# Performance work log

Hardware: AMD Instinct MI355X
Metric: run time of the kernel (lower is better)

The kernel has to match this reference:

```python
import jax, jax.numpy as jnp
import numpy as np

# FP8 E4M3 format constants
FP8_MAX = 448.0          # largest representable magnitude in E4M3
MANT_BITS = 3            # mantissa bits
_TINY = 2.0 ** -24


def fp8_fake_quant(x):
    """Per-tensor dynamic-scale FP8 (E4M3) fake quantization with STE.

    amax tracking (single-entry history on first call) -> scale = FP8_MAX/amax,
    scale, clamp to format range, round mantissa to MANT_BITS, dequantize.
    """
    amax = jax.lax.stop_gradient(jnp.max(jnp.abs(x)))
    scale = FP8_MAX / jnp.maximum(amax, _TINY)
    xs = jnp.clip(x * scale, -FP8_MAX, FP8_MAX)
    a = jnp.abs(xs)
    # exponent of each value; floor(log2) gives the binade, lsb is the quantum
    e = jnp.floor(jnp.log2(jnp.maximum(a, _TINY)))
    lsb = jnp.exp2(e - MANT_BITS)
    q = jnp.round(xs / lsb) * lsb
    q = jnp.where(a == 0.0, 0.0, q) / scale
    # straight-through estimator: forward q, backward identity
    return x + jax.lax.stop_gradient(q - x)


def setup_inputs() -> dict:
    key = jax.random.key(0)
    k1, k2, k3 = jax.random.split(key, 3)
    tokens, d_in, d_out = 4096, 4096, 16384
    x = jax.random.normal(k1, (tokens, d_in), dtype=jnp.float32)
    weight = jax.random.normal(k2, (d_out, d_in), dtype=jnp.float32) * 0.02
    bias = jax.random.normal(k3, (d_out,), dtype=jnp.float32) * 0.02
    return {"x": x, "weight": weight, "bias": bias}


def reference(x, weight, bias):
    qw = fp8_fake_quant(weight)          # quantize weights
    qx = fp8_fake_quant(x)               # quantize_input=True
    # F.linear: x @ W^T + b
    return jnp.einsum("ti,oi->to", qx, qw) + bias
```

## Files before the change

### kernel.cpp

```cpp
#include <hip/hip_runtime.h>
#include <hip/hip_bf16.h>


typedef __attribute__((ext_vector_type(8))) __bf16 bf16x8;
typedef __attribute__((ext_vector_type(4))) float f32x4;
typedef __attribute__((ext_vector_type(4))) unsigned int u32x4;

#define FP8_MAX 448.0f
#define TINY 5.9604644775390625e-8f

__device__ __forceinline__ void gload_lds16(const void* g, void* l) {
  __builtin_amdgcn_global_load_lds(
      (__attribute__((address_space(1))) void*)g,
      (__attribute__((address_space(3))) void*)l, 16, 0, 0);
}

__global__ __launch_bounds__(256) void amax_kernel(
    const float* __restrict__ in, long n, unsigned* __restrict__ out) {
  long i0 = (long)blockIdx.x * blockDim.x + threadIdx.x;
  long stride = (long)gridDim.x * blockDim.x;
  long n4 = n >> 2;
  const float4* in4 = (const float4*)in;
  float m = 0.f;
  for (long i = i0; i < n4; i += stride) {
    float4 v = in4[i];
    m = fmaxf(m, fmaxf(fmaxf(fabsf(v.x), fabsf(v.y)),
                       fmaxf(fabsf(v.z), fabsf(v.w))));
  }
  #pragma unroll
  for (int off = 32; off > 0; off >>= 1)
    m = fmaxf(m, __shfl_xor(m, off, 64));
  __shared__ float red[4];
  int lane = threadIdx.x & 63, wid = threadIdx.x >> 6;
  if (lane == 0) red[wid] = m;
  __syncthreads();
  if (threadIdx.x == 0) {
    m = fmaxf(fmaxf(red[0], red[1]), fmaxf(red[2], red[3]));
    atomicMax(out, __float_as_uint(m));
  }
}

__device__ __forceinline__ unsigned fq1(float x, float s) {
  float xs = x * s;
  xs = fminf(fmaxf(xs, -FP8_MAX), FP8_MAX);
  unsigned u = __float_as_uint(xs);
  unsigned sign = u & 0x80000000u;
  unsigned mag = u & 0x7fffffffu;
  unsigned r = (mag + 0x7FFFFu + ((mag >> 20) & 1u)) & 0xFFF00000u;
  return (sign | r) >> 16;
}

__global__ __launch_bounds__(256) void quant_kernel(
    const float* __restrict__ in, unsigned short* __restrict__ out,
    const unsigned* __restrict__ amaxp, long n) {
  float s = FP8_MAX / fmaxf(__uint_as_float(*amaxp), TINY);
  long i0 = (long)blockIdx.x * blockDim.x + threadIdx.x;
  long stride = (long)gridDim.x * blockDim.x;
  long n8 = n >> 3;
  const float4* in4 = (const float4*)in;
  u32x4* out8 = (u32x4*)out;
  for (long i = i0; i < n8; i += stride) {
    float4 v0 = in4[2 * i];
    float4 v1 = in4[2 * i + 1];
    u32x4 o;
    o.x = fq1(v0.x, s) | (fq1(v0.y, s) << 16);
    o.y = fq1(v0.z, s) | (fq1(v0.w, s) << 16);
    o.z = fq1(v1.x, s) | (fq1(v1.y, s) << 16);
    o.w = fq1(v1.z, s) | (fq1(v1.w, s) << 16);
    out8[i] = o;
  }
}

__global__ __launch_bounds__(512, 2) void gemm_kernel(
    const unsigned short* __restrict__ qx, const unsigned short* __restrict__ qw,
    const float* __restrict__ bias, const unsigned* __restrict__ amaxp,
    float* __restrict__ out, int M, int N, int K) {
  __shared__ unsigned short As[2][2][256 * 32];
  __shared__ unsigned short Bs[2][2][256 * 32];

  const int tid = threadIdx.x;
  const int lane = tid & 63;
  const int wid = tid >> 6;
  const int wr = wid >> 2;
  const int wc = wid & 3;

  const int nbn = N >> 8;
  const int cpx = gridDim.x >> 3;
  const int swz = (blockIdx.x & 7) * cpx + (blockIdx.x >> 3);
  const int bm0 = (swz / nbn) << 8;
  const int bn0 = (swz % nbn) << 8;

  f32x4 acc[8][4] = {};

  const int srow = tid >> 2;
  const int scb = ((tid & 3) * 16) ^ ((srow & 3) << 4);
  const size_t a_off = (size_t)(bm0 + srow) * K + (scb >> 1);
  const size_t b_off = (size_t)(bn0 + srow) * K + (scb >> 1);
  const size_t jstride = (size_t)128 * K;
  const int ldsb = wid * 1024;

  const int rcb = (((lane >> 4) << 4) ^ ((lane & 3) << 4)) >> 1;
  const int arb = (wr * 128 + (lane & 15)) * 32 + rcb;
  const int brb = (wc * 64 + (lane & 15)) * 32 + rcb;

#define STAGE(d, kh, kt)                                                   \
  {                                                                        \
    const unsigned short* ga = qx + a_off + (kt) + (kh) * 32;              \
    const unsigned short* gb = qw + b_off + (kt) + (kh) * 32;              \
    char* la = (char*)&As[d][kh][0] + ldsb;                                \
    char* lb = (char*)&Bs[d][kh][0] + ldsb;                                \
    gload_lds16(ga, la);                                                   \
    gload_lds16(ga + jstride, la + 8192);                                  \
    gload_lds16(gb, lb);                                                   \
    gload_lds16(gb + jstride, lb + 8192);                                  \
  }

#define PHASE(d, kh)                                                       \
  {                                                                        \
    bf16x8 a[8], b[4];                                                     \
    _Pragma("unroll")                                                      \
    for (int m = 0; m < 8; ++m)                                            \
      a[m] = __builtin_bit_cast(bf16x8,                                    \
                *(const u32x4*)&As[d][kh][arb + m * 512]);                 \
    _Pragma("unroll")                                                      \
    for (int n = 0; n < 4; ++n)                                            \
      b[n] = __builtin_bit_cast(bf16x8,                                    \
                *(const u32x4*)&Bs[d][kh][brb + n * 512]);                 \
    __builtin_amdgcn_s_setprio(1);                                         \
    _Pragma("unroll")                                                      \
    for (int m = 0; m < 8; ++m)                                            \
      _Pragma("unroll")                                                    \
      for (int n = 0; n < 4; ++n)                                          \
        acc[m][n] = __builtin_amdgcn_mfma_f32_16x16x32_bf16(               \
            a[m], b[n], acc[m][n], 0, 0, 0);                               \
    __builtin_amdgcn_s_setprio(0);                                         \
  }

  STAGE(0, 0, 0);
  STAGE(0, 1, 0);

  const int nt = K >> 6;
  int cur = 0;
  for (int t = 0; t < nt; ++t) {
    const int ktn = (t + 1 == nt) ? 0 : ((t + 1) << 6);
    STAGE(cur ^ 1, 0, ktn);
    asm volatile("s_waitcnt vmcnt(8)" ::: "memory");
    __builtin_amdgcn_s_barrier();
    PHASE(cur, 0);
    STAGE(cur ^ 1, 1, ktn);
    asm volatile("s_waitcnt vmcnt(8)" ::: "memory");
    __builtin_amdgcn_s_barrier();
    PHASE(cur, 1);
    __builtin_amdgcn_s_barrier();
    cur ^= 1;
  }

  const float ax = fmaxf(__uint_as_float(amaxp[0]), TINY);
  const float aw = fmaxf(__uint_as_float(amaxp[1]), TINY);
  const float inv = ax * aw * (1.0f / (FP8_MAX * FP8_MAX));
  const int col0 = bn0 + wc * 64 + (lane & 15);
  const int row0 = bm0 + wr * 128 + ((lane >> 4) << 2);
  #pragma unroll
  for (int n = 0; n < 4; ++n) {
    float bv = bias[col0 + n * 16];
    #pragma unroll
    for (int m = 0; m < 8; ++m)
      #pragma unroll
      for (int j = 0; j < 4; ++j)
        out[(size_t)(row0 + m * 16 + j) * N + col0 + n * 16] =
            acc[m][n][j] * inv + bv;
  }
#undef STAGE
#undef PHASE
}

extern "C" void kernel_launch(void* const* d_in, const int* in_sizes, int n_in,
                              void* d_out, int out_size, void* d_ws, size_t ws_size,
                              hipStream_t stream) {
  const float* x = (const float*)d_in[0];
  const float* w = (const float*)d_in[1];
  const float* bias = (const float*)d_in[2];
  float* out = (float*)d_out;

  long nx = in_sizes[0];
  long nw = in_sizes[1];
  int N = in_sizes[2];
  int K = (int)(nw / N);
  int M = (int)(nx / K);

  unsigned* amax = (unsigned*)d_ws;
  unsigned short* qx = (unsigned short*)((char*)d_ws + 256);
  unsigned short* qw = (unsigned short*)((char*)d_ws + 256 + (size_t)M * K * 2);

  hipMemsetAsync(d_ws, 0, 256, stream);
  amax_kernel<<<2048, 256, 0, stream>>>(x, nx, amax + 0);
  amax_kernel<<<2048, 256, 0, stream>>>(w, nw, amax + 1);
  quant_kernel<<<4096, 256, 0, stream>>>(x, qx, amax + 0, nx);
  quant_kernel<<<4096, 256, 0, stream>>>(w, qw, amax + 1, nw);

  int nwg = (M >> 8) * (N >> 8);
  gemm_kernel<<<nwg, 512, 0, stream>>>(qx, qw, bias, amax, out, M, N, K);
}
```

Measured before the change: 1.210 ms.

## Retune LDS XOR swizzle, drop trailing loop barrier, merge amax and quant launches

```diff
diff --git a/kernel.cpp b/kernel.cpp
--- a/kernel.cpp
+++ b/kernel.cpp
@@ -16,10 +16,19 @@
 }
 
 __global__ __launch_bounds__(256) void amax_kernel(
-    const float* __restrict__ in, long n, unsigned* __restrict__ out) {
-  long i0 = (long)blockIdx.x * blockDim.x + threadIdx.x;
-  long stride = (long)gridDim.x * blockDim.x;
-  long n4 = n >> 2;
+    const float* __restrict__ x, long nx, const float* __restrict__ w, long nw,
+    unsigned* __restrict__ out) {
+  const int xblocks = 512;
+  const float* in;
+  long n4;
+  int bid, nb, slot;
+  if (blockIdx.x < xblocks) {
+    in = x; n4 = nx >> 2; bid = blockIdx.x; nb = xblocks; slot = 0;
+  } else {
+    in = w; n4 = nw >> 2; bid = blockIdx.x - xblocks; nb = gridDim.x - xblocks; slot = 1;
+  }
+  long i0 = (long)bid * blockDim.x + threadIdx.x;
+  long stride = (long)nb * blockDim.x;
   const float4* in4 = (const float4*)in;
   float m = 0.f;
   for (long i = i0; i < n4; i += stride) {
@@ -36,7 +45,7 @@
   __syncthreads();
   if (threadIdx.x == 0) {
     m = fmaxf(fmaxf(red[0], red[1]), fmaxf(red[2], red[3]));
-    atomicMax(out, __float_as_uint(m));
+    atomicMax(out + slot, __float_as_uint(m));
   }
 }
 
@@ -51,12 +60,20 @@
 }
 
 __global__ __launch_bounds__(256) void quant_kernel(
-    const float* __restrict__ in, unsigned short* __restrict__ out,
-    const unsigned* __restrict__ amaxp, long n) {
-  float s = FP8_MAX / fmaxf(__uint_as_float(*amaxp), TINY);
-  long i0 = (long)blockIdx.x * blockDim.x + threadIdx.x;
-  long stride = (long)gridDim.x * blockDim.x;
-  long n8 = n >> 3;
+    const float* __restrict__ x, unsigned short* __restrict__ qx, long nx,
+    const float* __restrict__ w, unsigned short* __restrict__ qw, long nw,
+    const unsigned* __restrict__ amaxp) {
+  const int xblocks = 1024;
+  const float* in; unsigned short* out; long n8; int bid, nb, slot;
+  if (blockIdx.x < xblocks) {
+    in = x; out = qx; n8 = nx >> 3; bid = blockIdx.x; nb = xblocks; slot = 0;
+  } else {
+    in = w; out = qw; n8 = nw >> 3; bid = blockIdx.x - xblocks;
+    nb = gridDim.x - xblocks; slot = 1;
+  }
+  float s = FP8_MAX / fmaxf(__uint_as_float(amaxp[slot]), TINY);
+  long i0 = (long)bid * blockDim.x + threadIdx.x;
+  long stride = (long)nb * blockDim.x;
   const float4* in4 = (const float4*)in;
   u32x4* out8 = (u32x4*)out;
   for (long i = i0; i < n8; i += stride) {
@@ -93,13 +110,13 @@
   f32x4 acc[8][4] = {};
 
   const int srow = tid >> 2;
-  const int scb = ((tid & 3) * 16) ^ ((srow & 3) << 4);
+  const int scb = ((tid & 3) ^ ((srow >> 1) & 3)) << 4;
   const size_t a_off = (size_t)(bm0 + srow) * K + (scb >> 1);
   const size_t b_off = (size_t)(bn0 + srow) * K + (scb >> 1);
   const size_t jstride = (size_t)128 * K;
   const int ldsb = wid * 1024;
 
-  const int rcb = (((lane >> 4) << 4) ^ ((lane & 3) << 4)) >> 1;
+  const int rcb = ((((lane >> 4) ^ ((lane >> 1) & 3)) << 4) >> 1);
   const int arb = (wr * 128 + (lane & 15)) * 32 + rcb;
   const int brb = (wc * 64 + (lane & 15)) * 32 + rcb;
 
@@ -151,7 +168,6 @@
     asm volatile("s_waitcnt vmcnt(8)" ::: "memory");
     __builtin_amdgcn_s_barrier();
     PHASE(cur, 1);
-    __builtin_amdgcn_s_barrier();
     cur ^= 1;
   }
 
@@ -193,10 +209,8 @@
   unsigned short* qw = (unsigned short*)((char*)d_ws + 256 + (size_t)M * K * 2);
 
   hipMemsetAsync(d_ws, 0, 256, stream);
-  amax_kernel<<<2048, 256, 0, stream>>>(x, nx, amax + 0);
-  amax_kernel<<<2048, 256, 0, stream>>>(w, nw, amax + 1);
-  quant_kernel<<<4096, 256, 0, stream>>>(x, qx, amax + 0, nx);
-  quant_kernel<<<4096, 256, 0, stream>>>(w, qw, amax + 1, nw);
+  amax_kernel<<<2560, 256, 0, stream>>>(x, nx, w, nw, amax);
+  quant_kernel<<<5120, 256, 0, stream>>>(x, qx, nx, w, qw, nw, amax);
 
   int nwg = (M >> 8) * (N >> 8);
   gemm_kernel<<<nwg, 512, 0, stream>>>(qx, qw, bias, amax, out, M, N, K);
```

Result: faster. 1.107 ms (-8.5%).
